# Kernel optimization log

Hardware: AMD Instinct MI355X
Metric: run time of the kernel (lower is better)

The kernel has to match this reference:

```python
import jax, jax.numpy as jnp
import numpy as np

N_NODES = 100000

def _norm_coeffs(edge_index, n_nodes):
    # PyG GCNConv default: add self-loops, symmetric normalization D^-1/2 A D^-1/2
    src = jnp.concatenate([edge_index[0], jnp.arange(n_nodes, dtype=edge_index.dtype)])
    dst = jnp.concatenate([edge_index[1], jnp.arange(n_nodes, dtype=edge_index.dtype)])
    deg = jax.ops.segment_sum(jnp.ones_like(dst, dtype=jnp.float32), dst, num_segments=n_nodes)
    dinv = jnp.where(deg > 0, jax.lax.rsqrt(deg), 0.0)
    norm = dinv[src] * dinv[dst]  # [E + N]
    return src, dst, norm

def _gcn_conv(x, W, b, src, dst, norm, n_nodes):
    h = x @ W                       # [N, out] dense transform first (PyG order)
    msg = h[src] * norm[:, None]    # gather + scale, [E+N, out]
    out = jax.ops.segment_sum(msg, dst, num_segments=n_nodes)  # scatter-add aggregate
    return out + b

def setup_inputs() -> dict:
    key = jax.random.key(0)
    ks = jax.random.split(key, 8)
    in_feats, h_feats, num_classes = 128, 128, 64
    n_edges = 1_600_000
    x = jax.random.normal(ks[0], (N_NODES, in_feats), dtype=jnp.float32)
    edge_index = jax.random.randint(ks[1], (2, n_edges), 0, N_NODES, dtype=jnp.int64)
    def glorot(k, fi, fo):
        s = jnp.sqrt(6.0 / (fi + fo))
        return jax.random.uniform(k, (fi, fo), jnp.float32, -s, s)
    return {
        "x": x,
        "edge_index": edge_index,
        "W0": glorot(ks[2], in_feats, h_feats), "b0": jnp.zeros((h_feats,), jnp.float32),
        "W1": glorot(ks[3], h_feats, h_feats), "b1": jnp.zeros((h_feats,), jnp.float32),
        "W2": glorot(ks[4], h_feats, num_classes), "b2": jnp.zeros((num_classes,), jnp.float32),
    }

def reference(x, edge_index, W0, b0, W1, b1, W2, b2):
    n_nodes = x.shape[0]
    src, dst, norm = _norm_coeffs(edge_index, n_nodes)
    # layer 0 + 1: ReLU between (dropout is identity in eval mode)
    h = jax.nn.relu(_gcn_conv(x, W0, b0, src, dst, norm, n_nodes))
    h = jax.nn.relu(_gcn_conv(h, W1, b1, src, dst, norm, n_nodes))
    # final layer: no activation
    return _gcn_conv(h, W2, b2, src, dst, norm, n_nodes)
```

## Files before the change

### kernel.cpp

```cpp
#include <hip/hip_runtime.h>
#include <hip/hip_bf16.h>
#include <stdint.h>


typedef __attribute__((ext_vector_type(8))) short bf16x8;
typedef __attribute__((ext_vector_type(4))) float f32x4;

__device__ __forceinline__ float bflo(uint32_t u) { return __uint_as_float(u << 16); }
__device__ __forceinline__ float bfhi(uint32_t u) { return __uint_as_float(u & 0xffff0000u); }
__device__ __forceinline__ unsigned short f2bf(float f) {
    uint32_t x = __float_as_uint(f);
    return (unsigned short)((x + 0x7fffu + ((x >> 16) & 1u)) >> 16);
}

#define CE   4096
#define BINW 256

__global__ __launch_bounds__(256) void k_binhist(const int* __restrict__ dst,
                                                 int* __restrict__ cnt,
                                                 int NBIN, int E) {
    extern __shared__ int h[];
    int c = blockIdx.x, base = c * CE;
    for (int i = threadIdx.x; i < NBIN; i += 256) h[i] = 0;
    __syncthreads();
    for (int i = 0; i < CE; i += 256) {
        int e = base + i + threadIdx.x;
        if (e < E) atomicAdd(&h[dst[e] >> 8], 1);
    }
    __syncthreads();
    for (int i = threadIdx.x; i < NBIN; i += 256) cnt[c * NBIN + i] = h[i];
}

__global__ __launch_bounds__(256) void k_colscan(const int* __restrict__ cnt,
                                                 int* __restrict__ off_cb,
                                                 int* __restrict__ tot,
                                                 int NBIN, int NCHUNK) {
    __shared__ int part[256];
    int b = blockIdx.x, t = threadIdx.x;
    int K = (NCHUNK + 255) >> 8;
    int c0 = t * K;
    int vals[16];
    int s = 0;
    for (int k = 0; k < K; ++k) {
        int c = c0 + k;
        int v = (c < NCHUNK) ? cnt[c * NBIN + b] : 0;
        vals[k] = s;
        s += v;
    }
    part[t] = s;
    __syncthreads();
    for (int off = 1; off < 256; off <<= 1) {
        int x = (t >= off) ? part[t - off] : 0;
        __syncthreads();
        part[t] += x;
        __syncthreads();
    }
    int run = (t == 0) ? 0 : part[t - 1];
    for (int k = 0; k < K; ++k) {
        int c = c0 + k;
        if (c < NCHUNK) off_cb[c * NBIN + b] = run + vals[k];
    }
    if (t == 255) tot[b] = part[255];
}

__global__ __launch_bounds__(512) void k_binoff(const int* __restrict__ tot,
                                                int* __restrict__ bin_off,
                                                int* __restrict__ row_ptr,
                                                unsigned short* __restrict__ hzero,
                                                int NBIN, int N, int E) {
    __shared__ int part[512];
    int t = threadIdx.x;
    int v = (t < NBIN) ? tot[t] : 0;
    part[t] = v;
    __syncthreads();
    for (int off = 1; off < 512; off <<= 1) {
        int x = (t >= off) ? part[t - off] : 0;
        __syncthreads();
        part[t] += x;
        __syncthreads();
    }
    if (t < NBIN) bin_off[t] = part[t] - v;
    if (t == 0) { bin_off[NBIN] = E; row_ptr[N] = E; }
    if (t < 16) { uint4 z; z.x = z.y = z.z = z.w = 0; ((uint4*)hzero)[t] = z; }
}

__global__ __launch_bounds__(256) void k_binscatter(const int* __restrict__ src,
                                                    const int* __restrict__ dst,
                                                    const int* __restrict__ off_cb,
                                                    const int* __restrict__ bin_off,
                                                    unsigned int* __restrict__ bpack,
                                                    int NBIN, int E) {
    extern __shared__ int lcur[];
    int c = blockIdx.x, base = c * CE;
    for (int i = threadIdx.x; i < NBIN; i += 256)
        lcur[i] = off_cb[c * NBIN + i] + bin_off[i];
    __syncthreads();
    for (int i = 0; i < CE; i += 256) {
        int e = base + i + threadIdx.x;
        if (e < E) {
            int d = dst[e], s = src[e];
            int pos = atomicAdd(&lcur[d >> 8], 1);
            bpack[pos] = (unsigned)s | ((unsigned)(d & 255) << 24);
        }
    }
}

__global__ __launch_bounds__(256) void k_bindeg(const unsigned int* __restrict__ bpack,
                                                const int* __restrict__ bin_off,
                                                int* __restrict__ row_ptr,
                                                float* __restrict__ dinv, int N) {
    __shared__ int h[256];
    __shared__ int part[256];
    int b = blockIdx.x, t = threadIdx.x;
    int lo = b * BINW;
    h[t] = 0;
    __syncthreads();
    int s0 = bin_off[b], s1 = bin_off[b + 1];
    for (int i = s0 + t; i < s1; i += 256)
        atomicAdd(&h[bpack[i] >> 24], 1);
    __syncthreads();
    int dg = h[t];
    part[t] = dg;
    __syncthreads();
    for (int off = 1; off < 256; off <<= 1) {
        int x = (t >= off) ? part[t - off] : 0;
        __syncthreads();
        part[t] += x;
        __syncthreads();
    }
    if (lo + t < N) {
        row_ptr[lo + t] = s0 + part[t] - dg;
        dinv[lo + t] = rsqrtf((float)(dg + 1));
    }
}

__global__ __launch_bounds__(256) void k_csr(const unsigned int* __restrict__ bpack,
                                             const int* __restrict__ bin_off,
                                             const int* __restrict__ row_ptr,
                                             int* __restrict__ col_idx, int N) {
    __shared__ int lcur[256];
    int b = blockIdx.x, t = threadIdx.x;
    int lo = b * BINW;
    lcur[t] = (lo + t < N) ? row_ptr[lo + t] : 0;
    __syncthreads();
    int s0 = bin_off[b], s1 = bin_off[b + 1];
    for (int i = s0 + t; i < s1; i += 256) {
        unsigned pk = bpack[i];
        int pos = atomicAdd(&lcur[pk >> 24], 1);
        col_idx[pos] = (int)(pk & 0xFFFFFFu);
    }
}

__global__ __launch_bounds__(256) void k_prepw(const float* __restrict__ W0,
                                               const float* __restrict__ W1,
                                               const float* __restrict__ W2,
                                               unsigned short* __restrict__ wt0,
                                               unsigned short* __restrict__ wt1,
                                               unsigned short* __restrict__ wt2) {
    int id = blockIdx.x * 256 + threadIdx.x;
    const float* Wsrc;
    unsigned short* dst;
    int t, M, plane;
    if (id < 16384)      { t = id;         Wsrc = W0; dst = wt0; M = 128; plane = 16384; }
    else if (id < 32768) { t = id - 16384; Wsrc = W1; dst = wt1; M = 128; plane = 16384; }
    else if (id < 40960) { t = id - 32768; Wsrc = W2; dst = wt2; M = 64;  plane = 8192;  }
    else return;
    int k = (M == 128) ? (t >> 7) : (t >> 6);
    int c = (M == 128) ? (t & 127) : (t & 63);
    float v = Wsrc[k * M + c];
    unsigned short hi = f2bf(v);
    float lov = v - bflo((uint32_t)hi);
    dst[c * 128 + k]         = hi;
    dst[plane + c * 128 + k] = f2bf(lov);
}

template <int NCOL>
__global__ __launch_bounds__(256) void k_gemm_mfma(
    const float* __restrict__ A, const unsigned short* __restrict__ Wt,
    const float* __restrict__ dinv, unsigned short* __restrict__ H, int N) {
    constexpr int K = 128, KT = 64;
    constexpr int A_PLANE = 128 * KT;
    constexpr int W_PLANE = NCOL * KT;
    __shared__ __align__(16) unsigned short sm[2 * A_PLANE + 2 * W_PLANE];
    unsigned short* Ah  = sm;
    unsigned short* Al  = sm + A_PLANE;
    unsigned short* Whp = sm + 2 * A_PLANE;
    unsigned short* Wlp = sm + 2 * A_PLANE + W_PLANE;

    const int tid = threadIdx.x;
    const long r0 = (long)blockIdx.x * 128;
    const int w = tid >> 6, l = tid & 63;
    const int lr = l & 15, lk = l >> 4;
    constexpr int WR = (NCOL == 128) ? 4 : 2;
    const int wrow = (NCOL == 128) ? (w >> 1) * 64 : w * 32;
    const int wcol = (NCOL == 128) ? (w & 1) * 64 : 0;

    f32x4 acc[WR][4];
#pragma unroll
    for (int i = 0; i < WR; ++i)
#pragma unroll
        for (int j = 0; j < 4; ++j) acc[i][j] = (f32x4){0.f, 0.f, 0.f, 0.f};

    for (int kt = 0; kt < 2; ++kt) {
        if (kt) __syncthreads();
#pragma unroll
        for (int it = 0; it < 4; ++it) {
            int id = it * 256 + tid;
            int r = id >> 3, kc = id & 7;
            long gr = r0 + r;
            if (gr >= N) gr = N - 1;
            const float* ap = &A[gr * K + kt * KT + kc * 8];
            float4 v0 = *(const float4*)ap;
            float4 v1 = *(const float4*)(ap + 4);
            float vv[8] = {v0.x, v0.y, v0.z, v0.w, v1.x, v1.y, v1.z, v1.w};
            union { unsigned short u[8]; bf16x8 v; } ph, pl;
#pragma unroll
            for (int j = 0; j < 8; ++j) {
                unsigned short h = f2bf(vv[j]);
                ph.u[j] = h;
                pl.u[j] = f2bf(vv[j] - bflo((uint32_t)h));
            }
            int boff = r * 128 + ((kc * 16) ^ ((r & 7) << 4));
            *(bf16x8*)((char*)Ah + boff) = ph.v;
            *(bf16x8*)((char*)Al + boff) = pl.v;
        }
#pragma unroll
        for (int it = 0; it < NCOL / 32; ++it) {
            int id = it * 256 + tid;
            int c = id >> 3, kc = id & 7;
            const unsigned short* wp = &Wt[c * K + kt * KT + kc * 8];
            bf16x8 vh = *(const bf16x8*)wp;
            bf16x8 vl = *(const bf16x8*)(wp + NCOL * K);
            int boff = c * 128 + ((kc * 16) ^ ((c & 7) << 4));
            *(bf16x8*)((char*)Whp + boff) = vh;
            *(bf16x8*)((char*)Wlp + boff) = vl;
        }
        __syncthreads();
#pragma unroll
        for (int ks = 0; ks < 2; ++ks) {
            int kb = ks * 64 + lk * 16;
            bf16x8 bh[4], bl[4];
#pragma unroll
            for (int cf = 0; cf < 4; ++cf) {
                int c = wcol + cf * 16 + lr;
                int off = c * 128 + (kb ^ ((c & 7) << 4));
                bh[cf] = *(bf16x8*)((char*)Whp + off);
                bl[cf] = *(bf16x8*)((char*)Wlp + off);
            }
#pragma unroll
            for (int rf = 0; rf < WR; ++rf) {
                int r = wrow + rf * 16 + lr;
                int off = r * 128 + (kb ^ ((r & 7) << 4));
                bf16x8 ah = *(bf16x8*)((char*)Ah + off);
                bf16x8 al = *(bf16x8*)((char*)Al + off);
#pragma unroll
                for (int cf = 0; cf < 4; ++cf) {
                    acc[rf][cf] = __builtin_amdgcn_mfma_f32_16x16x32_bf16(ah, bh[cf], acc[rf][cf], 0, 0, 0);
                    acc[rf][cf] = __builtin_amdgcn_mfma_f32_16x16x32_bf16(al, bh[cf], acc[rf][cf], 0, 0, 0);
                    acc[rf][cf] = __builtin_amdgcn_mfma_f32_16x16x32_bf16(ah, bl[cf], acc[rf][cf], 0, 0, 0);
                }
            }
        }
    }
#pragma unroll
    for (int rf = 0; rf < WR; ++rf) {
        long rb = r0 + wrow + rf * 16 + lk * 4;
#pragma unroll
        for (int reg = 0; reg < 4; ++reg) {
            long r = rb + reg;
            if (r < N) {
                float dv = dinv[r];
#pragma unroll
                for (int cf = 0; cf < 4; ++cf) {
                    int c = wcol + cf * 16 + lr;
                    H[r * NCOL + c] = f2bf(dv * acc[rf][cf][reg]);
                }
            }
        }
    }
}

template <int F, bool RELU>
__global__ __launch_bounds__(256) void k_agg(const unsigned short* __restrict__ H,
                                             const int* __restrict__ row_ptr,
                                             const int* __restrict__ col_idx,
                                             const float* __restrict__ dinv,
                                             const float* __restrict__ bias,
                                             float* __restrict__ Y, int N) {
    constexpr int FL = F / 32;
    int lane = threadIdx.x & 63;
    int node = blockIdx.x * 4 + (threadIdx.x >> 6);
    if (node >= N) return;
    const int half = lane >> 5, hl = lane & 31;
    const int DUMMY = (F == 128) ? N : 2 * N;

    float acc[FL];
    if constexpr (F == 128) {
        if (half == 0) {
            uint64_t u = *(const uint64_t*)&H[(size_t)node * 128 + hl * 4];
            acc[0] = bflo((uint32_t)u);         acc[1] = bfhi((uint32_t)u);
            acc[2] = bflo((uint32_t)(u >> 32)); acc[3] = bfhi((uint32_t)(u >> 32));
        } else { acc[0] = acc[1] = acc[2] = acc[3] = 0.f; }
    } else {
        if (half == 0) {
            uint32_t u = *(const uint32_t*)&H[(size_t)node * 64 + hl * 2];
            acc[0] = bflo(u); acc[1] = bfhi(u);
        } else { acc[0] = acc[1] = 0.f; }
    }

    int start = row_ptr[node], end = row_ptr[node + 1];
    for (int base = start; base < end; base += 64) {
        int idx = DUMMY;
        if (base + lane < end) idx = col_idx[base + lane];
        int cnt = min(64, end - base);
        for (int j = 0; j < cnt; j += 8) {
            int s0 = __shfl(idx, j + half);
            int s1 = __shfl(idx, j + 2 + half);
            int s2 = __shfl(idx, j + 4 + half);
            int s3 = __shfl(idx, j + 6 + half);
            if constexpr (F == 128) {
                uint64_t u0 = *(const uint64_t*)&H[(size_t)s0 * 128 + hl * 4];
                uint64_t u1 = *(const uint64_t*)&H[(size_t)s1 * 128 + hl * 4];
                uint64_t u2 = *(const uint64_t*)&H[(size_t)s2 * 128 + hl * 4];
                uint64_t u3 = *(const uint64_t*)&H[(size_t)s3 * 128 + hl * 4];
                acc[0] += bflo((uint32_t)u0);         acc[1] += bfhi((uint32_t)u0);
                acc[2] += bflo((uint32_t)(u0 >> 32)); acc[3] += bfhi((uint32_t)(u0 >> 32));
                acc[0] += bflo((uint32_t)u1);         acc[1] += bfhi((uint32_t)u1);
                acc[2] += bflo((uint32_t)(u1 >> 32)); acc[3] += bfhi((uint32_t)(u1 >> 32));
                acc[0] += bflo((uint32_t)u2);         acc[1] += bfhi((uint32_t)u2);
                acc[2] += bflo((uint32_t)(u2 >> 32)); acc[3] += bfhi((uint32_t)(u2 >> 32));
                acc[0] += bflo((uint32_t)u3);         acc[1] += bfhi((uint32_t)u3);
                acc[2] += bflo((uint32_t)(u3 >> 32)); acc[3] += bfhi((uint32_t)(u3 >> 32));
            } else {
                uint32_t u0 = *(const uint32_t*)&H[(size_t)s0 * 64 + hl * 2];
                uint32_t u1 = *(const uint32_t*)&H[(size_t)s1 * 64 + hl * 2];
                uint32_t u2 = *(const uint32_t*)&H[(size_t)s2 * 64 + hl * 2];
                uint32_t u3 = *(const uint32_t*)&H[(size_t)s3 * 64 + hl * 2];
                acc[0] += bflo(u0); acc[1] += bfhi(u0);
                acc[0] += bflo(u1); acc[1] += bfhi(u1);
                acc[0] += bflo(u2); acc[1] += bfhi(u2);
                acc[0] += bflo(u3); acc[1] += bfhi(u3);
            }
        }
    }

    float part[FL];
#pragma unroll
    for (int f = 0; f < FL; ++f) part[f] = __shfl_xor(acc[f], 32);
    if (half == 0) {
        float dv = dinv[node];
        if constexpr (F == 128) {
            float4 b = *(const float4*)&bias[hl * 4];
            float4 o;
            o.x = dv * (acc[0] + part[0]) + b.x;
            o.y = dv * (acc[1] + part[1]) + b.y;
            o.z = dv * (acc[2] + part[2]) + b.z;
            o.w = dv * (acc[3] + part[3]) + b.w;
            if (RELU) {
                o.x = fmaxf(o.x, 0.f); o.y = fmaxf(o.y, 0.f);
                o.z = fmaxf(o.z, 0.f); o.w = fmaxf(o.w, 0.f);
            }
            *(float4*)&Y[(size_t)node * 128 + hl * 4] = o;
        } else {
            float2 b = *(const float2*)&bias[hl * 2];
            float2 o;
            o.x = dv * (acc[0] + part[0]) + b.x;
            o.y = dv * (acc[1] + part[1]) + b.y;
            if (RELU) { o.x = fmaxf(o.x, 0.f); o.y = fmaxf(o.y, 0.f); }
            *(float2*)&Y[(size_t)node * 64 + hl * 2] = o;
        }
    }
}

extern "C" void kernel_launch(void* const* d_in, const int* in_sizes, int n_in,
                              void* d_out, int out_size, void* d_ws, size_t ws_size,
                              hipStream_t stream) {
    const float* x  = (const float*)d_in[0];
    const int* eidx = (const int*)d_in[1];
    const float* W0 = (const float*)d_in[2];
    const float* b0 = (const float*)d_in[3];
    const float* W1 = (const float*)d_in[4];
    const float* b1 = (const float*)d_in[5];
    const float* W2 = (const float*)d_in[6];
    const float* b2 = (const float*)d_in[7];
    float* out = (float*)d_out;

    const int N = in_sizes[0] / 128;
    const int E = in_sizes[1] / 2;
    const int* srcp = eidx;
    const int* dstp = eidx + E;

    const int NBIN   = (N + BINW - 1) / BINW;
    const int NCHUNK = (E + CE - 1) / CE;

    char* p = (char*)d_ws;
    auto take = [&](size_t bytes) {
        char* r = p;
        p += (bytes + 255) & ~(size_t)255;
        return r;
    };
    int*            cnt     = (int*)take((size_t)NCHUNK * NBIN * 4);
    int*            off_cb  = (int*)take((size_t)NCHUNK * NBIN * 4);
    int*            tot     = (int*)take((size_t)NBIN * 4);
    int*            bin_off = (int*)take((size_t)(NBIN + 1) * 4);
    unsigned int*   bpack   = (unsigned int*)take((size_t)E * 4);
    int*            row_ptr = (int*)take((size_t)(N + 1) * 4);
    float*          dinv    = (float*)take((size_t)N * 4);
    int*            col_idx = (int*)take((size_t)E * 4);
    unsigned short* hbuf    = (unsigned short*)take((size_t)(N + 1) * 128 * 2);
    float*          ybuf    = (float*)take((size_t)N * 128 * 4);
    unsigned short* wt0     = (unsigned short*)take((size_t)2 * 16384 * 2);
    unsigned short* wt1     = (unsigned short*)take((size_t)2 * 16384 * 2);
    unsigned short* wt2     = (unsigned short*)take((size_t)2 * 8192 * 2);

    k_binhist<<<NCHUNK, 256, NBIN * 4, stream>>>(dstp, cnt, NBIN, E);
    k_prepw<<<160, 256, 0, stream>>>(W0, W1, W2, wt0, wt1, wt2);
    k_colscan<<<NBIN, 256, 0, stream>>>(cnt, off_cb, tot, NBIN, NCHUNK);
    k_binoff<<<1, 512, 0, stream>>>(tot, bin_off, row_ptr,
                                    hbuf + (size_t)N * 128, NBIN, N, E);
    k_binscatter<<<NCHUNK, 256, NBIN * 4, stream>>>(srcp, dstp, off_cb, bin_off,
                                                    bpack, NBIN, E);
    k_bindeg<<<NBIN, 256, 0, stream>>>(bpack, bin_off, row_ptr, dinv, N);
    k_csr<<<NBIN, 256, 0, stream>>>(bpack, bin_off, row_ptr, col_idx, N);

    int gemm_grid = (N + 127) / 128;
    int agg_grid  = (N + 3) / 4;

    k_gemm_mfma<128><<<gemm_grid, 256, 0, stream>>>(x, wt0, dinv, hbuf, N);
    k_agg<128, true><<<agg_grid, 256, 0, stream>>>(hbuf, row_ptr, col_idx,
                                                   dinv, b0, ybuf, N);
    k_gemm_mfma<128><<<gemm_grid, 256, 0, stream>>>(ybuf, wt1, dinv, hbuf, N);
    k_agg<128, true><<<agg_grid, 256, 0, stream>>>(hbuf, row_ptr, col_idx,
                                                   dinv, b1, ybuf, N);
    k_gemm_mfma<64><<<gemm_grid, 256, 0, stream>>>(ybuf, wt2, dinv, hbuf, N);
    k_agg<64, false><<<agg_grid, 256, 0, stream>>>(hbuf, row_ptr, col_idx,
                                                   dinv, b2, out, N);
}
```

Measured before the change: 394.9 us.

## Store hidden activations as bf16 and widen aggregation gathers to 16-byte loads

The aggregation kernel now writes intermediate layer outputs as bf16 instead of fp32, and the following GEMMs read the bf16 activations directly. This drops the hi/lo split and one of the three MFMA passes for those layers. The aggregation gather is restructured so each lane loads 8 bf16 values with a uint4 load, covering several edges per wavefront, followed by a shuffle reduction. This cuts activation memory traffic and GEMM compute, at the cost of rounding intermediate activations to bf16.

```diff
diff --git a/kernel.cpp b/kernel.cpp
--- a/kernel.cpp
+++ b/kernel.cpp
@@ -174,18 +174,19 @@
     dst[plane + c * 128 + k] = f2bf(lov);
 }
 
-template <int NCOL>
+template <int NCOL, bool BF16A>
 __global__ __launch_bounds__(256) void k_gemm_mfma(
-    const float* __restrict__ A, const unsigned short* __restrict__ Wt,
+    const void* __restrict__ Av, const unsigned short* __restrict__ Wt,
     const float* __restrict__ dinv, unsigned short* __restrict__ H, int N) {
     constexpr int K = 128, KT = 64;
-    constexpr int A_PLANE = 128 * KT;
+    constexpr int A_SH = 128 * KT;
+    constexpr int APL = BF16A ? 1 : 2;
     constexpr int W_PLANE = NCOL * KT;
-    __shared__ __align__(16) unsigned short sm[2 * A_PLANE + 2 * W_PLANE];
+    __shared__ __align__(16) unsigned short sm[APL * A_SH + 2 * W_PLANE];
     unsigned short* Ah  = sm;
-    unsigned short* Al  = sm + A_PLANE;
-    unsigned short* Whp = sm + 2 * A_PLANE;
-    unsigned short* Wlp = sm + 2 * A_PLANE + W_PLANE;
+    unsigned short* Al  = sm + A_SH;
+    unsigned short* Whp = sm + APL * A_SH;
+    unsigned short* Wlp = sm + APL * A_SH + W_PLANE;
 
     const int tid = threadIdx.x;
     const long r0 = (long)blockIdx.x * 128;
@@ -209,20 +210,26 @@
             int r = id >> 3, kc = id & 7;
             long gr = r0 + r;
             if (gr >= N) gr = N - 1;
-            const float* ap = &A[gr * K + kt * KT + kc * 8];
-            float4 v0 = *(const float4*)ap;
-            float4 v1 = *(const float4*)(ap + 4);
-            float vv[8] = {v0.x, v0.y, v0.z, v0.w, v1.x, v1.y, v1.z, v1.w};
-            union { unsigned short u[8]; bf16x8 v; } ph, pl;
-#pragma unroll
-            for (int j = 0; j < 8; ++j) {
-                unsigned short h = f2bf(vv[j]);
-                ph.u[j] = h;
-                pl.u[j] = f2bf(vv[j] - bflo((uint32_t)h));
-            }
             int boff = r * 128 + ((kc * 16) ^ ((r & 7) << 4));
-            *(bf16x8*)((char*)Ah + boff) = ph.v;
-            *(bf16x8*)((char*)Al + boff) = pl.v;
+            if constexpr (BF16A) {
+                const unsigned short* ap =
+                    (const unsigned short*)Av + gr * K + kt * KT + kc * 8;
+                *(bf16x8*)((char*)Ah + boff) = *(const bf16x8*)ap;
+            } else {
+                const float* ap = (const float*)Av + gr * K + kt * KT + kc * 8;
+                float4 v0 = *(const float4*)ap;
+                float4 v1 = *(const float4*)(ap + 4);
+                float vv[8] = {v0.x, v0.y, v0.z, v0.w, v1.x, v1.y, v1.z, v1.w};
+                union { unsigned short u[8]; bf16x8 v; } ph, pl;
+#pragma unroll
+                for (int j = 0; j < 8; ++j) {
+                    unsigned short h = f2bf(vv[j]);
+                    ph.u[j] = h;
+                    pl.u[j] = f2bf(vv[j] - bflo((uint32_t)h));
+                }
+                *(bf16x8*)((char*)Ah + boff) = ph.v;
+                *(bf16x8*)((char*)Al + boff) = pl.v;
+            }
         }
 #pragma unroll
         for (int it = 0; it < NCOL / 32; ++it) {
@@ -252,12 +259,20 @@
                 int r = wrow + rf * 16 + lr;
                 int off = r * 128 + (kb ^ ((r & 7) << 4));
                 bf16x8 ah = *(bf16x8*)((char*)Ah + off);
-                bf16x8 al = *(bf16x8*)((char*)Al + off);
-#pragma unroll
-                for (int cf = 0; cf < 4; ++cf) {
-                    acc[rf][cf] = __builtin_amdgcn_mfma_f32_16x16x32_bf16(ah, bh[cf], acc[rf][cf], 0, 0, 0);
-                    acc[rf][cf] = __builtin_amdgcn_mfma_f32_16x16x32_bf16(al, bh[cf], acc[rf][cf], 0, 0, 0);
-                    acc[rf][cf] = __builtin_amdgcn_mfma_f32_16x16x32_bf16(ah, bl[cf], acc[rf][cf], 0, 0, 0);
+                if constexpr (BF16A) {
+#pragma unroll
+                    for (int cf = 0; cf < 4; ++cf) {
+                        acc[rf][cf] = __builtin_amdgcn_mfma_f32_16x16x32_bf16(ah, bh[cf], acc[rf][cf], 0, 0, 0);
+                        acc[rf][cf] = __builtin_amdgcn_mfma_f32_16x16x32_bf16(ah, bl[cf], acc[rf][cf], 0, 0, 0);
+                    }
+                } else {
+                    bf16x8 al = *(bf16x8*)((char*)Al + off);
+#pragma unroll
+                    for (int cf = 0; cf < 4; ++cf) {
+                        acc[rf][cf] = __builtin_amdgcn_mfma_f32_16x16x32_bf16(ah, bh[cf], acc[rf][cf], 0, 0, 0);
+                        acc[rf][cf] = __builtin_amdgcn_mfma_f32_16x16x32_bf16(al, bh[cf], acc[rf][cf], 0, 0, 0);
+                        acc[rf][cf] = __builtin_amdgcn_mfma_f32_16x16x32_bf16(ah, bl[cf], acc[rf][cf], 0, 0, 0);
+                    }
                 }
             }
         }
@@ -280,94 +295,113 @@
     }
 }
 
-template <int F, bool RELU>
+template <int F, bool RELU, bool OUTBF16>
 __global__ __launch_bounds__(256) void k_agg(const unsigned short* __restrict__ H,
                                              const int* __restrict__ row_ptr,
                                              const int* __restrict__ col_idx,
                                              const float* __restrict__ dinv,
                                              const float* __restrict__ bias,
-                                             float* __restrict__ Y, int N) {
-    constexpr int FL = F / 32;
+                                             void* __restrict__ Yv, int N) {
+    constexpr int LPR = F / 8;
+    constexpr int EPW = 64 / LPR;
     int lane = threadIdx.x & 63;
     int node = blockIdx.x * 4 + (threadIdx.x >> 6);
     if (node >= N) return;
-    const int half = lane >> 5, hl = lane & 31;
+    const int q  = lane / LPR;
+    const int ql = lane % LPR;
     const int DUMMY = (F == 128) ? N : 2 * N;
 
-    float acc[FL];
-    if constexpr (F == 128) {
-        if (half == 0) {
-            uint64_t u = *(const uint64_t*)&H[(size_t)node * 128 + hl * 4];
-            acc[0] = bflo((uint32_t)u);         acc[1] = bfhi((uint32_t)u);
-            acc[2] = bflo((uint32_t)(u >> 32)); acc[3] = bfhi((uint32_t)(u >> 32));
-        } else { acc[0] = acc[1] = acc[2] = acc[3] = 0.f; }
-    } else {
-        if (half == 0) {
-            uint32_t u = *(const uint32_t*)&H[(size_t)node * 64 + hl * 2];
-            acc[0] = bflo(u); acc[1] = bfhi(u);
-        } else { acc[0] = acc[1] = 0.f; }
-    }
+    float acc[8];
+#pragma unroll
+    for (int f = 0; f < 8; ++f) acc[f] = 0.f;
+    if (q == 0) {
+        uint4 u = *((const uint4*)(H + (size_t)node * F) + ql);
+        acc[0] = bflo(u.x); acc[1] = bfhi(u.x);
+        acc[2] = bflo(u.y); acc[3] = bfhi(u.y);
+        acc[4] = bflo(u.z); acc[5] = bfhi(u.z);
+        acc[6] = bflo(u.w); acc[7] = bfhi(u.w);
+    }
+
+#define ACC8(u)                                                         \
+    acc[0] += bflo(u.x); acc[1] += bfhi(u.x);                           \
+    acc[2] += bflo(u.y); acc[3] += bfhi(u.y);                           \
+    acc[4] += bflo(u.z); acc[5] += bfhi(u.z);                           \
+    acc[6] += bflo(u.w); acc[7] += bfhi(u.w);
 
     int start = row_ptr[node], end = row_ptr[node + 1];
     for (int base = start; base < end; base += 64) {
         int idx = DUMMY;
         if (base + lane < end) idx = col_idx[base + lane];
         int cnt = min(64, end - base);
-        for (int j = 0; j < cnt; j += 8) {
-            int s0 = __shfl(idx, j + half);
-            int s1 = __shfl(idx, j + 2 + half);
-            int s2 = __shfl(idx, j + 4 + half);
-            int s3 = __shfl(idx, j + 6 + half);
-            if constexpr (F == 128) {
-                uint64_t u0 = *(const uint64_t*)&H[(size_t)s0 * 128 + hl * 4];
-                uint64_t u1 = *(const uint64_t*)&H[(size_t)s1 * 128 + hl * 4];
-                uint64_t u2 = *(const uint64_t*)&H[(size_t)s2 * 128 + hl * 4];
-                uint64_t u3 = *(const uint64_t*)&H[(size_t)s3 * 128 + hl * 4];
-                acc[0] += bflo((uint32_t)u0);         acc[1] += bfhi((uint32_t)u0);
-                acc[2] += bflo((uint32_t)(u0 >> 32)); acc[3] += bfhi((uint32_t)(u0 >> 32));
-                acc[0] += bflo((uint32_t)u1);         acc[1] += bfhi((uint32_t)u1);
-                acc[2] += bflo((uint32_t)(u1 >> 32)); acc[3] += bfhi((uint32_t)(u1 >> 32));
-                acc[0] += bflo((uint32_t)u2);         acc[1] += bfhi((uint32_t)u2);
-                acc[2] += bflo((uint32_t)(u2 >> 32)); acc[3] += bfhi((uint32_t)(u2 >> 32));
-                acc[0] += bflo((uint32_t)u3);         acc[1] += bfhi((uint32_t)u3);
-                acc[2] += bflo((uint32_t)(u3 >> 32)); acc[3] += bfhi((uint32_t)(u3 >> 32));
-            } else {
-                uint32_t u0 = *(const uint32_t*)&H[(size_t)s0 * 64 + hl * 2];
-                uint32_t u1 = *(const uint32_t*)&H[(size_t)s1 * 64 + hl * 2];
-                uint32_t u2 = *(const uint32_t*)&H[(size_t)s2 * 64 + hl * 2];
-                uint32_t u3 = *(const uint32_t*)&H[(size_t)s3 * 64 + hl * 2];
-                acc[0] += bflo(u0); acc[1] += bfhi(u0);
-                acc[0] += bflo(u1); acc[1] += bfhi(u1);
-                acc[0] += bflo(u2); acc[1] += bfhi(u2);
-                acc[0] += bflo(u3); acc[1] += bfhi(u3);
-            }
-        }
-    }
-
-    float part[FL];
-#pragma unroll
-    for (int f = 0; f < FL; ++f) part[f] = __shfl_xor(acc[f], 32);
-    if (half == 0) {
-        float dv = dinv[node];
-        if constexpr (F == 128) {
-            float4 b = *(const float4*)&bias[hl * 4];
+        int j = 0;
+        for (; j + 4 * EPW <= cnt; j += 4 * EPW) {
+            int s0 = __shfl(idx, j + q);
+            int s1 = __shfl(idx, j + EPW + q);
+            int s2 = __shfl(idx, j + 2 * EPW + q);
+            int s3 = __shfl(idx, j + 3 * EPW + q);
+            uint4 u0 = *((const uint4*)(H + (size_t)s0 * F) + ql);
+            uint4 u1 = *((const uint4*)(H + (size_t)s1 * F) + ql);
+            uint4 u2 = *((const uint4*)(H + (size_t)s2 * F) + ql);
+            uint4 u3 = *((const uint4*)(H + (size_t)s3 * F) + ql);
+            ACC8(u0); ACC8(u1); ACC8(u2); ACC8(u3);
+        }
+        if (j + 2 * EPW <= cnt) {
+            int s0 = __shfl(idx, j + q);
+            int s1 = __shfl(idx, j + EPW + q);
+            uint4 u0 = *((const uint4*)(H + (size_t)s0 * F) + ql);
+            uint4 u1 = *((const uint4*)(H + (size_t)s1 * F) + ql);
+            ACC8(u0); ACC8(u1);
+            j += 2 * EPW;
+        }
+        for (; j < cnt; j += EPW) {
+            int s = __shfl(idx, j + q);
+            uint4 u = *((const uint4*)(H + (size_t)s * F) + ql);
+            ACC8(u);
+        }
+    }
+#undef ACC8
+
+#pragma unroll
+    for (int f = 0; f < 8; ++f) {
+        if constexpr (F == 64) acc[f] += __shfl_xor(acc[f], 8);
+        acc[f] += __shfl_xor(acc[f], 16);
+        acc[f] += __shfl_xor(acc[f], 32);
+    }
+
+    float dv = dinv[node];
+    if constexpr (OUTBF16) {
+        if (q == 0) {
+            float4 b0 = *(const float4*)&bias[ql * 8];
+            float4 b1 = *(const float4*)&bias[ql * 8 + 4];
+            float y[8];
+            y[0] = dv * acc[0] + b0.x; y[1] = dv * acc[1] + b0.y;
+            y[2] = dv * acc[2] + b0.z; y[3] = dv * acc[3] + b0.w;
+            y[4] = dv * acc[4] + b1.x; y[5] = dv * acc[5] + b1.y;
+            y[6] = dv * acc[6] + b1.z; y[7] = dv * acc[7] + b1.w;
+            uint4 o;
+            unsigned* ow = (unsigned*)&o;
+#pragma unroll
+            for (int k = 0; k < 4; ++k) {
+                float a0 = y[2 * k], a1 = y[2 * k + 1];
+                if (RELU) { a0 = fmaxf(a0, 0.f); a1 = fmaxf(a1, 0.f); }
+                ow[k] = (unsigned)f2bf(a0) | ((unsigned)f2bf(a1) << 16);
+            }
+            *((uint4*)((unsigned short*)Yv + (size_t)node * F) + ql) = o;
+        }
+    } else {
+        if (q < 2) {
+            int fb = ql * 8 + q * 4;
+            float4 b = *(const float4*)&bias[fb];
             float4 o;
-            o.x = dv * (acc[0] + part[0]) + b.x;
-            o.y = dv * (acc[1] + part[1]) + b.y;
-            o.z = dv * (acc[2] + part[2]) + b.z;
-            o.w = dv * (acc[3] + part[3]) + b.w;
+            o.x = dv * acc[q * 4 + 0] + b.x;
+            o.y = dv * acc[q * 4 + 1] + b.y;
+            o.z = dv * acc[q * 4 + 2] + b.z;
+            o.w = dv * acc[q * 4 + 3] + b.w;
             if (RELU) {
                 o.x = fmaxf(o.x, 0.f); o.y = fmaxf(o.y, 0.f);
                 o.z = fmaxf(o.z, 0.f); o.w = fmaxf(o.w, 0.f);
             }
-            *(float4*)&Y[(size_t)node * 128 + hl * 4] = o;
-        } else {
-            float2 b = *(const float2*)&bias[hl * 2];
-            float2 o;
-            o.x = dv * (acc[0] + part[0]) + b.x;
-            o.y = dv * (acc[1] + part[1]) + b.y;
-            if (RELU) { o.x = fmaxf(o.x, 0.f); o.y = fmaxf(o.y, 0.f); }
-            *(float2*)&Y[(size_t)node * 64 + hl * 2] = o;
+            *(float4*)((float*)Yv + (size_t)node * F + fb) = o;
         }
     }
 }
@@ -408,7 +442,7 @@
     float*          dinv    = (float*)take((size_t)N * 4);
     int*            col_idx = (int*)take((size_t)E * 4);
     unsigned short* hbuf    = (unsigned short*)take((size_t)(N + 1) * 128 * 2);
-    float*          ybuf    = (float*)take((size_t)N * 128 * 4);
+    unsigned short* ybuf    = (unsigned short*)take((size_t)N * 128 * 2);
     unsigned short* wt0     = (unsigned short*)take((size_t)2 * 16384 * 2);
     unsigned short* wt1     = (unsigned short*)take((size_t)2 * 16384 * 2);
     unsigned short* wt2     = (unsigned short*)take((size_t)2 * 8192 * 2);
@@ -426,13 +460,13 @@
     int gemm_grid = (N + 127) / 128;
     int agg_grid  = (N + 3) / 4;
 
-    k_gemm_mfma<128><<<gemm_grid, 256, 0, stream>>>(x, wt0, dinv, hbuf, N);
-    k_agg<128, true><<<agg_grid, 256, 0, stream>>>(hbuf, row_ptr, col_idx,
-                                                   dinv, b0, ybuf, N);
-    k_gemm_mfma<128><<<gemm_grid, 256, 0, stream>>>(ybuf, wt1, dinv, hbuf, N);
-    k_agg<128, true><<<agg_grid, 256, 0, stream>>>(hbuf, row_ptr, col_idx,
-                                                   dinv, b1, ybuf, N);
-    k_gemm_mfma<64><<<gemm_grid, 256, 0, stream>>>(ybuf, wt2, dinv, hbuf, N);
-    k_agg<64, false><<<agg_grid, 256, 0, stream>>>(hbuf, row_ptr, col_idx,
-                                                   dinv, b2, out, N);
-}
+    k_gemm_mfma<128, false><<<gemm_grid, 256, 0, stream>>>(x, wt0, dinv, hbuf, N);
+    k_agg<128, true, true><<<agg_grid, 256, 0, stream>>>(hbuf, row_ptr, col_idx,
+                                                         dinv, b0, ybuf, N);
+    k_gemm_mfma<128, true><<<gemm_grid, 256, 0, stream>>>(ybuf, wt1, dinv, hbuf, N);
+    k_agg<128, true, true><<<agg_grid, 256, 0, stream>>>(hbuf, row_ptr, col_idx,
+                                                         dinv, b1, ybuf, N);
+    k_gemm_mfma<64, true><<<gemm_grid, 256, 0, stream>>>(ybuf, wt2, dinv, hbuf, N);
+    k_agg<64, false, false><<<agg_grid, 256, 0, stream>>>(hbuf, row_ptr, col_idx,
+                                                          dinv, b2, out, N);
+}
```

New measurement: 366.9 us. 1.08x faster.
